# Kernel tuning notes

Measured on AMD Instinct MI355X. Metric: run time of the kernel, lower is better.

The kernel has to match this reference:

```python
import jax, jax.numpy as jnp
import numpy as np

TOPK = 20

def setup_inputs() -> dict:
    key = jax.random.key(0)
    k1, k2, k3 = jax.random.split(key, 3)
    B, n, D = 4, 4096, 256
    src1 = jax.random.normal(k1, (B, n, D), dtype=jnp.float32)
    src2 = jax.random.normal(k2, (B, n, D), dtype=jnp.float32)
    memoryMartix = jax.random.normal(k3, (n, n), dtype=jnp.float32)
    return {"src1": src1, "src2": src2, "memoryMartix": memoryMartix}

def reference(src1, src2, memoryMartix):
    # softmax over dim=1 of the [n, n] memory matrix
    probs = jax.nn.softmax(memoryMartix, axis=1)            # [n, n]
    # top-k along dim=1: values and indices per row
    vtopk, ind = jax.lax.top_k(probs, TOPK)                 # [n, k], [n, k]
    # gather src2 rows per output position: [B, n, k, D]
    gathered = jnp.take(src2, ind, axis=1)
    # weighted sum over the k selected neighbors
    src = jnp.einsum('bnkd,nk->bnd', gathered, vtopk)       # [B, n, D]
    return src + src1
```

## Files before the change

### kernel.cpp

```cpp
#include <hip/hip_runtime.h>
#include <math.h>

#define TOPK  20
#define NROW  4096
#define DDIM  256
#define NB    4
#define WPB   4
#define BLOCK (WPB * 64)
#define NCHUNK 16

struct WaveScratch {
    float cand_v[64];
    int   cand_i[64];
    float w[TOPK];
    int   idx[TOPK];
};

__device__ __forceinline__ void wave_lds_fence() {
    asm volatile("s_waitcnt lgkmcnt(0)" ::: "memory");
}

__device__ __forceinline__ bool lex_gt(float av, int ai, float bv, int bi) {
    return (av > bv) || (av == bv && ai < bi);
}

__device__ __forceinline__ void bitonic64_desc(float& v, int& i, int lane) {
#pragma unroll
    for (int k = 2; k <= 64; k <<= 1) {
#pragma unroll
        for (int j = k >> 1; j > 0; j >>= 1) {
            float pv = __shfl_xor(v, j, 64);
            int   pi = __shfl_xor(i, j, 64);
            bool takeBig = ((lane & k) == 0) == ((lane & j) == 0);
            bool pBig = lex_gt(pv, pi, v, i);
            if (takeBig == pBig) { v = pv; i = pi; }
        }
    }
}

__global__ __launch_bounds__(BLOCK, 4) void fused_topk_gather(
    const float* __restrict__ src1,
    const float* __restrict__ src2,
    const float* __restrict__ mem,
    float* __restrict__ out)
{
    __shared__ WaveScratch ws_all[WPB];
    const int wave = threadIdx.x >> 6;
    const int lane = threadIdx.x & 63;
    const int n    = blockIdx.x * WPB + wave;
    WaveScratch& ws = ws_all[wave];

    const float4* mrow = (const float4*)(mem + (size_t)n * NROW);
    float4 v4[NCHUNK];
#pragma unroll
    for (int j = 0; j < NCHUNK; ++j) v4[j] = mrow[lane + 64 * j];

    float bv = -INFINITY; int bi = 0x7fffffff;
#pragma unroll
    for (int j = 0; j < NCHUNK; ++j) {
        const int base = 4 * lane + 256 * j;
        if (v4[j].x > bv) { bv = v4[j].x; bi = base + 0; }
        if (v4[j].y > bv) { bv = v4[j].y; bi = base + 1; }
        if (v4[j].z > bv) { bv = v4[j].z; bi = base + 2; }
        if (v4[j].w > bv) { bv = v4[j].w; bi = base + 3; }
    }

    float sv = bv; int si = bi;
    bitonic64_desc(sv, si, lane);
    const float rowmax = __shfl(sv, 0, 64);
    const float tv     = __shfl(sv, 19, 64);
    const int   ti     = __shfl(si, 19, 64);

    float lsum = 0.f;
#pragma unroll
    for (int j = 0; j < NCHUNK; ++j) {
        lsum += __expf(v4[j].x - rowmax) + __expf(v4[j].y - rowmax)
              + __expf(v4[j].z - rowmax) + __expf(v4[j].w - rowmax);
    }
#pragma unroll
    for (int o = 32; o > 0; o >>= 1) lsum += __shfl_xor(lsum, o, 64);
    const float inv_denom = 1.0f / lsum;

    int cnt = 0;
#pragma unroll
    for (int j = 0; j < NCHUNK; ++j) {
        const int base = 4 * lane + 256 * j;
        cnt += (v4[j].x > tv) || (v4[j].x == tv && (base + 0) <= ti);
        cnt += (v4[j].y > tv) || (v4[j].y == tv && (base + 1) <= ti);
        cnt += (v4[j].z > tv) || (v4[j].z == tv && (base + 2) <= ti);
        cnt += (v4[j].w > tv) || (v4[j].w == tv && (base + 3) <= ti);
    }
    int incl = cnt;
#pragma unroll
    for (int o = 1; o < 64; o <<= 1) {
        int t = __shfl_up(incl, o, 64);
        if (lane >= o) incl += t;
    }
    const int total = __builtin_amdgcn_readfirstlane(__shfl(incl, 63, 64));

    if (total <= 64) {
        int off = incl - cnt;
#pragma unroll
        for (int j = 0; j < NCHUNK; ++j) {
            const int base = 4 * lane + 256 * j;
            const float4 q = v4[j];
            if ((q.x > tv) || (q.x == tv && (base + 0) <= ti)) { ws.cand_v[off] = q.x; ws.cand_i[off] = base + 0; ++off; }
            if ((q.y > tv) || (q.y == tv && (base + 1) <= ti)) { ws.cand_v[off] = q.y; ws.cand_i[off] = base + 1; ++off; }
            if ((q.z > tv) || (q.z == tv && (base + 2) <= ti)) { ws.cand_v[off] = q.z; ws.cand_i[off] = base + 2; ++off; }
            if ((q.w > tv) || (q.w == tv && (base + 3) <= ti)) { ws.cand_v[off] = q.w; ws.cand_i[off] = base + 3; ++off; }
        }
        wave_lds_fence();
        float cv = -INFINITY; int ci = 0x7fffffff;
        if (lane < total) { cv = ws.cand_v[lane]; ci = ws.cand_i[lane]; }
        bitonic64_desc(cv, ci, lane);
        if (lane < TOPK) {
            ws.w[lane]   = __expf(cv - rowmax) * inv_denom;
            ws.idx[lane] = ci;
        }
    } else {
        unsigned long long dead = 0;
        float cv = bv; int ci = bi;
        for (int r = 0; r < TOPK; ++r) {
            float wv = cv; int wi = ci;
#pragma unroll
            for (int o = 32; o > 0; o >>= 1) {
                float ov = __shfl_xor(wv, o, 64);
                int   oi = __shfl_xor(wi, o, 64);
                if (lex_gt(ov, oi, wv, wi)) { wv = ov; wi = oi; }
            }
            if (lane == 0) {
                ws.w[r]   = __expf(wv - rowmax) * inv_denom;
                ws.idx[r] = wi;
            }
            if (ci == wi) {
                const int e = (((wi >> 8) & 15) << 2) | (wi & 3);
                dead |= (1ull << e);
                cv = -INFINITY; ci = 0x7fffffff;
#pragma unroll
                for (int j = 0; j < NCHUNK; ++j) {
                    const int base = 4 * lane + 256 * j;
                    if (!((dead >> (4 * j + 0)) & 1) && v4[j].x > cv) { cv = v4[j].x; ci = base + 0; }
                    if (!((dead >> (4 * j + 1)) & 1) && v4[j].y > cv) { cv = v4[j].y; ci = base + 1; }
                    if (!((dead >> (4 * j + 2)) & 1) && v4[j].z > cv) { cv = v4[j].z; ci = base + 2; }
                    if (!((dead >> (4 * j + 3)) & 1) && v4[j].w > cv) { cv = v4[j].w; ci = base + 3; }
                }
            }
        }
    }
    wave_lds_fence();

    float wk[TOPK]; int ik[TOPK];
#pragma unroll
    for (int k = 0; k < TOPK; ++k) { wk[k] = ws.w[k]; ik[k] = ws.idx[k]; }

    const float4* s1 = (const float4*)src1;
    const float4* s2 = (const float4*)src2;
    float4*       o4 = (float4*)out;
#pragma unroll
    for (int b = 0; b < NB; ++b) {
        const size_t rowbase = ((size_t)b * NROW + n) * (DDIM / 4) + lane;
        float4 acc = s1[rowbase];
#pragma unroll
        for (int k = 0; k < TOPK; ++k) {
            const float4 g = s2[((size_t)b * NROW + ik[k]) * (DDIM / 4) + lane];
            acc.x = fmaf(wk[k], g.x, acc.x);
            acc.y = fmaf(wk[k], g.y, acc.y);
            acc.z = fmaf(wk[k], g.z, acc.z);
            acc.w = fmaf(wk[k], g.w, acc.w);
        }
        o4[rowbase] = acc;
    }
}

extern "C" void kernel_launch(void* const* d_in, const int* in_sizes, int n_in,
                              void* d_out, int out_size, void* d_ws, size_t ws_size,
                              hipStream_t stream) {
    const float* src1 = (const float*)d_in[0];
    const float* src2 = (const float*)d_in[1];
    const float* mem  = (const float*)d_in[2];
    float* out = (float*)d_out;
    fused_topk_gather<<<NROW / WPB, BLOCK, 0, stream>>>(src1, src2, mem, out);
}
```

Before: 178.5 us.

## Stream memory row from global instead of holding it in registers; use LDS atomic compaction

Stops caching the 64-float memory-row slice per lane in registers. The row is now re-read from global/L2 on each pass (max scan, exp-sum plus candidate compaction, fallback rescans). The prefix-scan compaction becomes per-element LDS atomicAdd into a bounded candidate buffer, and block size drops to two waves. Gather weights and indices are read from LDS inside the loop instead of register arrays. The aim is lower VGPR pressure and higher occupancy, at the cost of repeated row reads and atomic contention. Candidate order from the atomics is nondeterministic, but the bitonic sort restores it.

```diff
diff --git a/kernel.cpp b/kernel.cpp
--- a/kernel.cpp
+++ b/kernel.cpp
@@ -5,7 +5,7 @@
 #define NROW  4096
 #define DDIM  256
 #define NB    4
-#define WPB   4
+#define WPB   2
 #define BLOCK (WPB * 64)
 #define NCHUNK 16
 
@@ -14,6 +14,7 @@
     int   cand_i[64];
     float w[TOPK];
     int   idx[TOPK];
+    int   cnt;
 };
 
 __device__ __forceinline__ void wave_lds_fence() {
@@ -50,19 +51,19 @@
     const int n    = blockIdx.x * WPB + wave;
     WaveScratch& ws = ws_all[wave];
 
+    if (lane == 0) ws.cnt = 0;
+
     const float4* mrow = (const float4*)(mem + (size_t)n * NROW);
-    float4 v4[NCHUNK];
-#pragma unroll
-    for (int j = 0; j < NCHUNK; ++j) v4[j] = mrow[lane + 64 * j];
 
     float bv = -INFINITY; int bi = 0x7fffffff;
-#pragma unroll
+#pragma unroll 4
     for (int j = 0; j < NCHUNK; ++j) {
+        const float4 q = mrow[lane + 64 * j];
         const int base = 4 * lane + 256 * j;
-        if (v4[j].x > bv) { bv = v4[j].x; bi = base + 0; }
-        if (v4[j].y > bv) { bv = v4[j].y; bi = base + 1; }
-        if (v4[j].z > bv) { bv = v4[j].z; bi = base + 2; }
-        if (v4[j].w > bv) { bv = v4[j].w; bi = base + 3; }
+        if (q.x > bv) { bv = q.x; bi = base + 0; }
+        if (q.y > bv) { bv = q.y; bi = base + 1; }
+        if (q.z > bv) { bv = q.z; bi = base + 2; }
+        if (q.w > bv) { bv = q.w; bi = base + 3; }
     }
 
     float sv = bv; int si = bi;
@@ -70,46 +71,40 @@
     const float rowmax = __shfl(sv, 0, 64);
     const float tv     = __shfl(sv, 19, 64);
     const int   ti     = __shfl(si, 19, 64);
+    wave_lds_fence();
 
     float lsum = 0.f;
-#pragma unroll
+#pragma unroll 4
     for (int j = 0; j < NCHUNK; ++j) {
-        lsum += __expf(v4[j].x - rowmax) + __expf(v4[j].y - rowmax)
-              + __expf(v4[j].z - rowmax) + __expf(v4[j].w - rowmax);
+        const float4 q = mrow[lane + 64 * j];
+        const int base = 4 * lane + 256 * j;
+        lsum += __expf(q.x - rowmax) + __expf(q.y - rowmax)
+              + __expf(q.z - rowmax) + __expf(q.w - rowmax);
+        if ((q.x > tv) || (q.x == tv && (base + 0) <= ti)) {
+            int off = atomicAdd(&ws.cnt, 1);
+            if (off < 64) { ws.cand_v[off] = q.x; ws.cand_i[off] = base + 0; }
+        }
+        if ((q.y > tv) || (q.y == tv && (base + 1) <= ti)) {
+            int off = atomicAdd(&ws.cnt, 1);
+            if (off < 64) { ws.cand_v[off] = q.y; ws.cand_i[off] = base + 1; }
+        }
+        if ((q.z > tv) || (q.z == tv && (base + 2) <= ti)) {
+            int off = atomicAdd(&ws.cnt, 1);
+            if (off < 64) { ws.cand_v[off] = q.z; ws.cand_i[off] = base + 2; }
+        }
+        if ((q.w > tv) || (q.w == tv && (base + 3) <= ti)) {
+            int off = atomicAdd(&ws.cnt, 1);
+            if (off < 64) { ws.cand_v[off] = q.w; ws.cand_i[off] = base + 3; }
+        }
     }
 #pragma unroll
     for (int o = 32; o > 0; o >>= 1) lsum += __shfl_xor(lsum, o, 64);
     const float inv_denom = 1.0f / lsum;
 
-    int cnt = 0;
-#pragma unroll
-    for (int j = 0; j < NCHUNK; ++j) {
-        const int base = 4 * lane + 256 * j;
-        cnt += (v4[j].x > tv) || (v4[j].x == tv && (base + 0) <= ti);
-        cnt += (v4[j].y > tv) || (v4[j].y == tv && (base + 1) <= ti);
-        cnt += (v4[j].z > tv) || (v4[j].z == tv && (base + 2) <= ti);
-        cnt += (v4[j].w > tv) || (v4[j].w == tv && (base + 3) <= ti);
-    }
-    int incl = cnt;
-#pragma unroll
-    for (int o = 1; o < 64; o <<= 1) {
-        int t = __shfl_up(incl, o, 64);
-        if (lane >= o) incl += t;
-    }
-    const int total = __builtin_amdgcn_readfirstlane(__shfl(incl, 63, 64));
+    wave_lds_fence();
+    const int total = ws.cnt;
 
     if (total <= 64) {
-        int off = incl - cnt;
-#pragma unroll
-        for (int j = 0; j < NCHUNK; ++j) {
-            const int base = 4 * lane + 256 * j;
-            const float4 q = v4[j];
-            if ((q.x > tv) || (q.x == tv && (base + 0) <= ti)) { ws.cand_v[off] = q.x; ws.cand_i[off] = base + 0; ++off; }
-            if ((q.y > tv) || (q.y == tv && (base + 1) <= ti)) { ws.cand_v[off] = q.y; ws.cand_i[off] = base + 1; ++off; }
-            if ((q.z > tv) || (q.z == tv && (base + 2) <= ti)) { ws.cand_v[off] = q.z; ws.cand_i[off] = base + 2; ++off; }
-            if ((q.w > tv) || (q.w == tv && (base + 3) <= ti)) { ws.cand_v[off] = q.w; ws.cand_i[off] = base + 3; ++off; }
-        }
-        wave_lds_fence();
         float cv = -INFINITY; int ci = 0x7fffffff;
         if (lane < total) { cv = ws.cand_v[lane]; ci = ws.cand_i[lane]; }
         bitonic64_desc(cv, ci, lane);
@@ -119,8 +114,17 @@
         }
     } else {
         unsigned long long dead = 0;
-        float cv = bv; int ci = bi;
         for (int r = 0; r < TOPK; ++r) {
+            float cv = -INFINITY; int ci = 0x7fffffff;
+#pragma unroll 4
+            for (int j = 0; j < NCHUNK; ++j) {
+                const float4 q = mrow[lane + 64 * j];
+                const int base = 4 * lane + 256 * j;
+                if (!((dead >> (4 * j + 0)) & 1) && q.x > cv) { cv = q.x; ci = base + 0; }
+                if (!((dead >> (4 * j + 1)) & 1) && q.y > cv) { cv = q.y; ci = base + 1; }
+                if (!((dead >> (4 * j + 2)) & 1) && q.z > cv) { cv = q.z; ci = base + 2; }
+                if (!((dead >> (4 * j + 3)) & 1) && q.w > cv) { cv = q.w; ci = base + 3; }
+            }
             float wv = cv; int wi = ci;
 #pragma unroll
             for (int o = 32; o > 0; o >>= 1) {
@@ -133,25 +137,12 @@
                 ws.idx[r] = wi;
             }
             if (ci == wi) {
-                const int e = (((wi >> 8) & 15) << 2) | (wi & 3);
+                const int e = 4 * ((wi >> 8) & 15) + (wi & 3);
                 dead |= (1ull << e);
-                cv = -INFINITY; ci = 0x7fffffff;
-#pragma unroll
-                for (int j = 0; j < NCHUNK; ++j) {
-                    const int base = 4 * lane + 256 * j;
-                    if (!((dead >> (4 * j + 0)) & 1) && v4[j].x > cv) { cv = v4[j].x; ci = base + 0; }
-                    if (!((dead >> (4 * j + 1)) & 1) && v4[j].y > cv) { cv = v4[j].y; ci = base + 1; }
-                    if (!((dead >> (4 * j + 2)) & 1) && v4[j].z > cv) { cv = v4[j].z; ci = base + 2; }
-                    if (!((dead >> (4 * j + 3)) & 1) && v4[j].w > cv) { cv = v4[j].w; ci = base + 3; }
-                }
             }
         }
     }
     wave_lds_fence();
-
-    float wk[TOPK]; int ik[TOPK];
-#pragma unroll
-    for (int k = 0; k < TOPK; ++k) { wk[k] = ws.w[k]; ik[k] = ws.idx[k]; }
 
     const float4* s1 = (const float4*)src1;
     const float4* s2 = (const float4*)src2;
@@ -162,11 +153,13 @@
         float4 acc = s1[rowbase];
 #pragma unroll
         for (int k = 0; k < TOPK; ++k) {
-            const float4 g = s2[((size_t)b * NROW + ik[k]) * (DDIM / 4) + lane];
-            acc.x = fmaf(wk[k], g.x, acc.x);
-            acc.y = fmaf(wk[k], g.y, acc.y);
-            acc.z = fmaf(wk[k], g.z, acc.z);
-            acc.w = fmaf(wk[k], g.w, acc.w);
+            const float wk = ws.w[k];
+            const int   ik = ws.idx[k];
+            const float4 g = s2[((size_t)b * NROW + ik) * (DDIM / 4) + lane];
+            acc.x = fmaf(wk, g.x, acc.x);
+            acc.y = fmaf(wk, g.y, acc.y);
+            acc.z = fmaf(wk, g.z, acc.z);
+            acc.w = fmaf(wk, g.w, acc.w);
         }
         o4[rowbase] = acc;
     }
```

After: 157.3 us. 1.13x faster.

## Split fused kernel into top-k select and batch-parallel gather kernels

Applied to the files above, without the earlier changes.

Splits the single fused kernel into two launches. The first computes the softmax top-k weights and indices with two waves per block and writes them to a global workspace. The second launches one block per row with one wave per batch, so the four batch gathers run in parallel instead of one after another inside a wave. This shortens the serial dependency chain and adds parallelism in the gather phase, at the cost of an extra launch and a round trip of the top-k results through global memory.

```diff
diff --git a/kernel.cpp b/kernel.cpp
--- a/kernel.cpp
+++ b/kernel.cpp
@@ -5,16 +5,11 @@
 #define NROW  4096
 #define DDIM  256
 #define NB    4
-#define WPB   4
-#define BLOCK (WPB * 64)
 #define NCHUNK 16
 
-struct WaveScratch {
-    float cand_v[64];
-    int   cand_i[64];
-    float w[TOPK];
-    int   idx[TOPK];
-};
+#define AWPB   2
+#define ABLOCK (AWPB * 64)
+#define BBLOCK 256
 
 __device__ __forceinline__ void wave_lds_fence() {
     asm volatile("s_waitcnt lgkmcnt(0)" ::: "memory");
@@ -38,17 +33,16 @@
     }
 }
 
-__global__ __launch_bounds__(BLOCK, 4) void fused_topk_gather(
-    const float* __restrict__ src1,
-    const float* __restrict__ src2,
+__global__ __launch_bounds__(ABLOCK, 4) void topk_select(
     const float* __restrict__ mem,
-    float* __restrict__ out)
+    float* __restrict__ ws_w,
+    int*   __restrict__ ws_i)
 {
-    __shared__ WaveScratch ws_all[WPB];
+    __shared__ float cand_v[AWPB][64];
+    __shared__ int   cand_i[AWPB][64];
     const int wave = threadIdx.x >> 6;
     const int lane = threadIdx.x & 63;
-    const int n    = blockIdx.x * WPB + wave;
-    WaveScratch& ws = ws_all[wave];
+    const int n    = blockIdx.x * AWPB + wave;
 
     const float4* mrow = (const float4*)(mem + (size_t)n * NROW);
     float4 v4[NCHUNK];
@@ -98,24 +92,27 @@
     }
     const int total = __builtin_amdgcn_readfirstlane(__shfl(incl, 63, 64));
 
+    float* gw = ws_w + (size_t)n * TOPK;
+    int*   gi = ws_i + (size_t)n * TOPK;
+
     if (total <= 64) {
         int off = incl - cnt;
 #pragma unroll
         for (int j = 0; j < NCHUNK; ++j) {
             const int base = 4 * lane + 256 * j;
             const float4 q = v4[j];
-            if ((q.x > tv) || (q.x == tv && (base + 0) <= ti)) { ws.cand_v[off] = q.x; ws.cand_i[off] = base + 0; ++off; }
-            if ((q.y > tv) || (q.y == tv && (base + 1) <= ti)) { ws.cand_v[off] = q.y; ws.cand_i[off] = base + 1; ++off; }
-            if ((q.z > tv) || (q.z == tv && (base + 2) <= ti)) { ws.cand_v[off] = q.z; ws.cand_i[off] = base + 2; ++off; }
-            if ((q.w > tv) || (q.w == tv && (base + 3) <= ti)) { ws.cand_v[off] = q.w; ws.cand_i[off] = base + 3; ++off; }
+            if ((q.x > tv) || (q.x == tv && (base + 0) <= ti)) { cand_v[wave][off] = q.x; cand_i[wave][off] = base + 0; ++off; }
+            if ((q.y > tv) || (q.y == tv && (base + 1) <= ti)) { cand_v[wave][off] = q.y; cand_i[wave][off] = base + 1; ++off; }
+            if ((q.z > tv) || (q.z == tv && (base + 2) <= ti)) { cand_v[wave][off] = q.z; cand_i[wave][off] = base + 2; ++off; }
+            if ((q.w > tv) || (q.w == tv && (base + 3) <= ti)) { cand_v[wave][off] = q.w; cand_i[wave][off] = base + 3; ++off; }
         }
         wave_lds_fence();
         float cv = -INFINITY; int ci = 0x7fffffff;
-        if (lane < total) { cv = ws.cand_v[lane]; ci = ws.cand_i[lane]; }
+        if (lane < total) { cv = cand_v[wave][lane]; ci = cand_i[wave][lane]; }
         bitonic64_desc(cv, ci, lane);
         if (lane < TOPK) {
-            ws.w[lane]   = __expf(cv - rowmax) * inv_denom;
-            ws.idx[lane] = ci;
+            gw[lane] = __expf(cv - rowmax) * inv_denom;
+            gi[lane] = ci;
         }
     } else {
         unsigned long long dead = 0;
@@ -129,11 +126,11 @@
                 if (lex_gt(ov, oi, wv, wi)) { wv = ov; wi = oi; }
             }
             if (lane == 0) {
-                ws.w[r]   = __expf(wv - rowmax) * inv_denom;
-                ws.idx[r] = wi;
+                gw[r] = __expf(wv - rowmax) * inv_denom;
+                gi[r] = wi;
             }
             if (ci == wi) {
-                const int e = (((wi >> 8) & 15) << 2) | (wi & 3);
+                const int e = 4 * ((wi >> 8) & 15) + (wi & 3);
                 dead |= (1ull << e);
                 cv = -INFINITY; ci = 0x7fffffff;
 #pragma unroll
@@ -147,29 +144,41 @@
             }
         }
     }
-    wave_lds_fence();
+}
 
+__global__ __launch_bounds__(BBLOCK, 4) void gather_epilogue(
+    const float* __restrict__ src1,
+    const float* __restrict__ src2,
+    const float* __restrict__ ws_w,
+    const int*   __restrict__ ws_i,
+    float* __restrict__ out)
+{
+    const int n    = blockIdx.x;
+    const int b    = threadIdx.x >> 6;
+    const int lane = threadIdx.x & 63;
+
+    const float* gw = ws_w + (size_t)n * TOPK;
+    const int*   gi = ws_i + (size_t)n * TOPK;
     float wk[TOPK]; int ik[TOPK];
 #pragma unroll
-    for (int k = 0; k < TOPK; ++k) { wk[k] = ws.w[k]; ik[k] = ws.idx[k]; }
+    for (int k = 0; k < TOPK; ++k) { wk[k] = gw[k]; ik[k] = gi[k]; }
 
     const float4* s1 = (const float4*)src1;
     const float4* s2 = (const float4*)src2;
     float4*       o4 = (float4*)out;
+
+    const size_t rowbase = ((size_t)b * NROW + n) * (DDIM / 4) + lane;
+    const size_t bbase   = (size_t)b * NROW * (DDIM / 4) + lane;
+    float4 acc = s1[rowbase];
 #pragma unroll
-    for (int b = 0; b < NB; ++b) {
-        const size_t rowbase = ((size_t)b * NROW + n) * (DDIM / 4) + lane;
-        float4 acc = s1[rowbase];
-#pragma unroll
-        for (int k = 0; k < TOPK; ++k) {
-            const float4 g = s2[((size_t)b * NROW + ik[k]) * (DDIM / 4) + lane];
-            acc.x = fmaf(wk[k], g.x, acc.x);
-            acc.y = fmaf(wk[k], g.y, acc.y);
-            acc.z = fmaf(wk[k], g.z, acc.z);
-            acc.w = fmaf(wk[k], g.w, acc.w);
-        }
-        o4[rowbase] = acc;
+    for (int k = 0; k < TOPK; ++k) {
+        const float4 g = s2[bbase + (size_t)ik[k] * (DDIM / 4)];
+        acc.x = fmaf(wk[k], g.x, acc.x);
+        acc.y = fmaf(wk[k], g.y, acc.y);
+        acc.z = fmaf(wk[k], g.z, acc.z);
+        acc.w = fmaf(wk[k], g.w, acc.w);
     }
+    o4[rowbase] = acc;
 }
 
 extern "C" void kernel_launch(void* const* d_in, const int* in_sizes, int n_in,
@@ -179,5 +188,10 @@
     const float* src2 = (const float*)d_in[1];
     const float* mem  = (const float*)d_in[2];
     float* out = (float*)d_out;
-    fused_topk_gather<<<NROW / WPB, BLOCK, 0, stream>>>(src1, src2, mem, out);
+
+    float* ws_w = (float*)d_ws;
+    int*   ws_i = (int*)d_ws + (size_t)NROW * TOPK;
+
+    topk_select<<<NROW / AWPB, ABLOCK, 0, stream>>>(mem, ws_w, ws_i);
+    gather_epilogue<<<NROW, BBLOCK, 0, stream>>>(src1, src2, ws_w, ws_i, out);
 }
```

New measurement: 170.0 us. -4.7%, faster.
